# Kernel tuning notes

Hardware: AMD Instinct MI355X
Metric: run time of the kernel (lower is better)

Reference implementation:

```python
import jax, jax.numpy as jnp
import numpy as np

HID = 2048   # hidden_size
NH = 32      # num_heads (== num_kv_heads)
HD = 64      # head_dim
TH, TW = 8, 16     # tile sizes (tile numel 128, flex-attention block)
WH, WW = 16, 32    # window sizes in tokens
SCALE = 1.0 / np.sqrt(HD)


def _kv_tile_index(h_dim, w_dim):
    # Static tile-level sliding window (mirrors sliding_window_tile_2d mask_mod).
    Ht, Wt = h_dim // TH, w_dim // TW          # tile grid
    wh, ww = WH // TH, WW // TW                # window in tile units
    lr, rr = wh // 2, wh // 2 + (wh % 2 - 1)
    lc, rc = ww // 2, ww // 2 + (ww % 2 - 1)
    cr = np.clip(np.arange(Ht), lr, Ht - 1 - rr)   # clamped window center rows
    cc = np.clip(np.arange(Wt), lc, Wt - 1 - rc)
    rows = cr[:, None] + np.arange(-lr, rr + 1)[None, :]   # [Ht, wh]
    cols = cc[:, None] + np.arange(-lc, rc + 1)[None, :]   # [Wt, ww]
    idx = rows[:, None, :, None] * Wt + cols[None, :, None, :]  # [Ht,Wt,wh,ww]
    return idx.reshape(Ht * Wt, wh * ww)


def _tile_order(x, h_dim, w_dim):
    # seq layout (nth th ntw tw) -> [B, NH, n_tiles, TH*TW, HD]  (the einops rearrange)
    B, S, _ = x.shape
    nth, ntw = h_dim // TH, w_dim // TW
    x = x.reshape(B, nth, TH, ntw, TW, NH, HD)
    x = x.transpose(0, 5, 1, 3, 2, 4, 6)  # b h nth ntw th tw d
    return x.reshape(B, NH, nth * ntw, TH * TW, HD)


def setup_inputs() -> dict:
    key = jax.random.key(0)
    ks = jax.random.split(key, 5)
    B, hd, wd = 2, 64, 64
    S = hd * wd
    sc = 1.0 / np.sqrt(HID)
    return {
        "hidden_states": jax.random.normal(ks[0], (B, S, HID), jnp.float32),
        "Wq": jax.random.normal(ks[1], (HID, NH * HD), jnp.float32) * sc,
        "Wk": jax.random.normal(ks[2], (HID, NH * HD), jnp.float32) * sc,
        "Wv": jax.random.normal(ks[3], (HID, NH * HD), jnp.float32) * sc,
        "Wo": jax.random.normal(ks[4], (NH * HD, HID), jnp.float32) * sc,
        "h_dim": hd,
        "w_dim": wd,
    }


def reference(hidden_states, Wq, Wk, Wv, Wo, h_dim, w_dim):
    B, S, _ = hidden_states.shape
    q = _tile_order(hidden_states @ Wq, h_dim, w_dim)
    k = _tile_order(hidden_states @ Wk, h_dim, w_dim)
    v = _tile_order(hidden_states @ Wv, h_dim, w_dim)
    kv_tiles = jnp.asarray(_kv_tile_index(h_dim, w_dim))  # [T, nw] static
    T, nw = kv_tiles.shape
    tn = TH * TW
    # gather the allowed kv tiles per query tile (block-sparse structure)
    kg = k[:, :, kv_tiles].reshape(B, NH, T, nw * tn, HD)
    vg = v[:, :, kv_tiles].reshape(B, NH, T, nw * tn, HD)
    s = jnp.einsum('bhtqd,bhtkd->bhtqk', q, kg) * SCALE  # [B,H,T,128,nw*128]
    p = jax.nn.softmax(s, axis=-1)
    o = jnp.einsum('bhtqk,bhtkd->bhtqd', p, vg)
    # back to (nth th ntw tw) token order, then output projection
    nth, ntw = h_dim // TH, w_dim // TW
    o = o.reshape(B, NH, nth, ntw, TH, TW, HD)
    o = o.transpose(0, 2, 4, 3, 5, 1, 6).reshape(B, S, NH * HD)
    return o @ Wo
```

## Files before the change

### kernel.cpp

```cpp
#include <hip/hip_runtime.h>
#include <math.h>

typedef _Float16 f16;
typedef _Float16 f16x2 __attribute__((ext_vector_type(2)));
typedef _Float16 f16x4 __attribute__((ext_vector_type(4)));
typedef _Float16 f16x8 __attribute__((ext_vector_type(8)));
typedef float f32x4 __attribute__((ext_vector_type(4)));

#define K_HID 2048
#define N_SEQ 4096
#define N_BATCH 2
#define M_ROWS 8192

__device__ __forceinline__ void gl2lds16(const f16* g, f16* l) {
  auto gp = (const __attribute__((address_space(1))) unsigned*)(unsigned long long)(uintptr_t)g;
  auto lp = (__attribute__((address_space(3))) unsigned*)(unsigned)(uintptr_t)l;
  __builtin_amdgcn_global_load_lds(gp, lp, 16, 0, 0);
}

__global__ __launch_bounds__(256) void cvt_f32_to_f16(const float* __restrict__ x,
                                                      f16* __restrict__ y, int n) {
  int i = (blockIdx.x * 256 + threadIdx.x) * 8;
  if (i >= n) return;
  float4 a = *(const float4*)(x + i);
  float4 b = *(const float4*)(x + i + 4);
  f16x8 o;
  o[0] = (f16)a.x; o[1] = (f16)a.y; o[2] = (f16)a.z; o[3] = (f16)a.w;
  o[4] = (f16)b.x; o[5] = (f16)b.y; o[6] = (f16)b.z; o[7] = (f16)b.w;
  *(f16x8*)(y + i) = o;
}

__global__ __launch_bounds__(256) void transpose_cvt(const float* __restrict__ W0,
                                                     const float* __restrict__ W1,
                                                     const float* __restrict__ W2,
                                                     const float* __restrict__ W3,
                                                     f16* __restrict__ WT) {
  const float* W = (blockIdx.z == 0) ? W0 : (blockIdx.z == 1) ? W1
                 : (blockIdx.z == 2) ? W2 : W3;
  f16* Wt = WT + (size_t)blockIdx.z * K_HID * K_HID;
  __shared__ float tile[32][33];
  int bx = blockIdx.x * 32;
  int by = blockIdx.y * 32;
  int x = threadIdx.x & 31;
  int y = threadIdx.x >> 5;
  for (int i = 0; i < 32; i += 8)
    tile[y + i][x] = W[(size_t)(by + y + i) * K_HID + bx + x];
  __syncthreads();
  for (int i = 0; i < 32; i += 8)
    Wt[(size_t)(bx + y + i) * K_HID + by + x] = (f16)tile[x][y + i];
}

template <typename OutT>
__global__ __launch_bounds__(512, 2) void gemm_bt(const f16* __restrict__ A,
                                                  const f16* __restrict__ BtBase,
                                                  OutT* __restrict__ CBase,
                                                  int M, int N, int Kd,
                                                  size_t bzStride, size_t czStride) {
  const f16* Bt = BtBase + bzStride * blockIdx.z;
  OutT* C = CBase + czStride * blockIdx.z;
  __shared__ f16 sA[2][256 * 64];
  __shared__ f16 sB[2][256 * 64];
  int tid = threadIdx.x;
  int lane = tid & 63, wave = tid >> 6;
  int quad = lane >> 4, l16 = lane & 15;
  int mBase = blockIdx.y * 256, nBase = blockIdx.x * 256;
  int wm = (wave >> 2) * 128, wn = (wave & 3) * 64;

  f32x4 acc[8][4];
#pragma unroll
  for (int mf = 0; mf < 8; mf++)
#pragma unroll
    for (int nf = 0; nf < 4; nf++) acc[mf][nf] = (f32x4){0.f, 0.f, 0.f, 0.f};

  int r8 = lane >> 3;
  int csw = ((lane & 7) ^ r8) * 8;
  const f16* Ag = A + (size_t)(mBase + wave * 32 + r8) * Kd + csw;
  const f16* Bg = Bt + (size_t)(nBase + wave * 32 + r8) * Kd + csw;

  f16* lA0 = &sA[0][wave * 2048];
  f16* lA1 = &sA[1][wave * 2048];
  f16* lB0 = &sB[0][wave * 2048];
  f16* lB1 = &sB[1][wave * 2048];

#define STAGE_A(dst, t)                                                  \
  { _Pragma("unroll") for (int q = 0; q < 4; ++q)                        \
      gl2lds16(Ag + (size_t)(q * 8) * Kd + (size_t)(t) * 64, (dst) + q * 512); }
#define STAGE_B(dst, t)                                                  \
  { _Pragma("unroll") for (int q = 0; q < 4; ++q)                        \
      gl2lds16(Bg + (size_t)(q * 8) * Kd + (size_t)(t) * 64, (dst) + q * 512); }

  int aRow = (wm + l16) * 64;
  int bRow = (wn + l16) * 64;
  int c0 = (quad ^ (l16 & 7)) * 8;
  int c1 = c0 ^ 32;

  const int NT = Kd >> 6;
  STAGE_A(lA0, 0);
  STAGE_B(lB0, 0);

  const f16* sAc = &sA[0][0]; const f16* sAo = &sA[1][0];
  const f16* sBc = &sB[0][0]; const f16* sBo = &sB[1][0];
  f16* lAn = lA1; f16* lAo = lA0;
  f16* lBn = lB1; f16* lBo = lB0;

  for (int t = 0; t < NT; ++t) {
    if (t + 1 < NT) {
      STAGE_A(lAn, t + 1);
      asm volatile("s_waitcnt vmcnt(4)" ::: "memory");
    } else {
      asm volatile("s_waitcnt vmcnt(0)" ::: "memory");
    }
    __builtin_amdgcn_s_barrier();
    __builtin_amdgcn_sched_barrier(0);

    f16x8 bf[4][2], af[4][2];
#pragma unroll
    for (int nf = 0; nf < 4; nf++) {
      bf[nf][0] = *(const f16x8*)&sBc[bRow + nf * 1024 + c0];
      bf[nf][1] = *(const f16x8*)&sBc[bRow + nf * 1024 + c1];
    }
#pragma unroll
    for (int mf = 0; mf < 4; mf++) {
      af[mf][0] = *(const f16x8*)&sAc[aRow + mf * 1024 + c0];
      af[mf][1] = *(const f16x8*)&sAc[aRow + mf * 1024 + c1];
    }
    __builtin_amdgcn_s_setprio(1);
#pragma unroll
    for (int mf = 0; mf < 4; mf++)
#pragma unroll
      for (int nf = 0; nf < 4; nf++) {
        acc[mf][nf] = __builtin_amdgcn_mfma_f32_16x16x32_f16(af[mf][0], bf[nf][0], acc[mf][nf], 0, 0, 0);
        acc[mf][nf] = __builtin_amdgcn_mfma_f32_16x16x32_f16(af[mf][1], bf[nf][1], acc[mf][nf], 0, 0, 0);
      }
    __builtin_amdgcn_s_setprio(0);

    if (t + 1 < NT) STAGE_B(lBn, t + 1);

#pragma unroll
    for (int mf = 0; mf < 4; mf++) {
      af[mf][0] = *(const f16x8*)&sAc[aRow + 4096 + mf * 1024 + c0];
      af[mf][1] = *(const f16x8*)&sAc[aRow + 4096 + mf * 1024 + c1];
    }
    __builtin_amdgcn_s_setprio(1);
#pragma unroll
    for (int mf = 0; mf < 4; mf++)
#pragma unroll
      for (int nf = 0; nf < 4; nf++) {
        acc[mf + 4][nf] = __builtin_amdgcn_mfma_f32_16x16x32_f16(af[mf][0], bf[nf][0], acc[mf + 4][nf], 0, 0, 0);
        acc[mf + 4][nf] = __builtin_amdgcn_mfma_f32_16x16x32_f16(af[mf][1], bf[nf][1], acc[mf + 4][nf], 0, 0, 0);
      }
    __builtin_amdgcn_s_setprio(0);
    __builtin_amdgcn_sched_barrier(0);
    __builtin_amdgcn_s_barrier();

    { const f16* tt;
      tt = sAc; sAc = sAo; sAo = tt;
      tt = sBc; sBc = sBo; sBo = tt; }
    { f16* tt;
      tt = lAn; lAn = lAo; lAo = tt;
      tt = lBn; lBn = lBo; lBo = tt; }
  }
#undef STAGE_A
#undef STAGE_B

#pragma unroll
  for (int mf = 0; mf < 8; mf++) {
    int row = mBase + wm + mf * 16 + quad * 4;
#pragma unroll
    for (int nf = 0; nf < 4; nf++) {
      int col = nBase + wn + nf * 16 + l16;
      OutT* Cp = C + (size_t)row * N + col;
#pragma unroll
      for (int r = 0; r < 4; r++) Cp[(size_t)r * N] = (OutT)acc[mf][nf][r];
    }
  }
}

__global__ __launch_bounds__(256) void attn_kernel(const f16* __restrict__ Q,
                                                   const f16* __restrict__ Kg,
                                                   const f16* __restrict__ V,
                                                   f16* __restrict__ O) {
  __shared__ f16 sK[64 * 72];
  __shared__ f16 sVt[64 * 72];
  __shared__ f16 sPt[128 * 72];

  int t = blockIdx.x, h = blockIdx.y, b = blockIdx.z;
  int nth_i = t >> 2, ntw_i = t & 3;
  int tid = threadIdx.x;
  int lane = tid & 63, wave = tid >> 6;
  int quad = lane >> 4, l16 = lane & 15;
  const size_t bstride = (size_t)N_SEQ * K_HID;
  const f16* Qb = Q + (size_t)b * bstride + h * 64;
  const f16* Kb = Kg + (size_t)b * bstride + h * 64;
  const f16* Vb = V + (size_t)b * bstride + h * 64;

  const float SC2 = 0.18033688f;

  for (int i = tid; i < 1024; i += 256) {
    int qr = i >> 3, dc = (i & 7) * 8;
    int s = (nth_i * 8 + (qr >> 4)) * 64 + ntw_i * 16 + (qr & 15);
    *(float4*)&sPt[qr * 72 + dc] = *(const float4*)&Qb[(size_t)s * K_HID + dc];
  }
  __syncthreads();

  f16x8 qf[2][2];
#pragma unroll
  for (int qs = 0; qs < 2; qs++)
#pragma unroll
    for (int kk = 0; kk < 2; kk++)
      qf[qs][kk] = *(const f16x8*)&sPt[(wave * 32 + qs * 16 + l16) * 72 + kk * 32 + quad * 8];

  f32x4 oacc[2][4];
#pragma unroll
  for (int qs = 0; qs < 2; qs++)
#pragma unroll
    for (int dt = 0; dt < 4; dt++) oacc[qs][dt] = (f32x4){0.f, 0.f, 0.f, 0.f};
  float mrow[2] = {-1e30f, -1e30f};
  float lrow[2] = {0.f, 0.f};

  int cr = min(max(nth_i, 1), 7);
  int cc = min(max(ntw_i, 1), 3);

  for (int c = 0; c < 8; c++) {
    int kt = c >> 1, half = c & 1;
    int ti = cr - 1 + (kt >> 1), tj = cc - 1 + (kt & 1);
    for (int i = tid; i < 512; i += 256) {
      int kl = i >> 3, dc = (i & 7) * 8;
      int kr = half * 64 + kl;
      int s = (ti * 8 + (kr >> 4)) * 64 + tj * 16 + (kr & 15);
      *(float4*)&sK[kl * 72 + dc] = *(const float4*)&Kb[(size_t)s * K_HID + dc];
    }
    {
      int pr = tid >> 3, dc = (tid & 7) * 8;
      int k0 = pr * 2;
      int kr0 = half * 64 + k0, kr1 = kr0 + 1;
      int s0 = (ti * 8 + (kr0 >> 4)) * 64 + tj * 16 + (kr0 & 15);
      int s1 = (ti * 8 + (kr1 >> 4)) * 64 + tj * 16 + (kr1 & 15);
      f16x8 v0 = *(const f16x8*)&Vb[(size_t)s0 * K_HID + dc];
      f16x8 v1 = *(const f16x8*)&Vb[(size_t)s1 * K_HID + dc];
      int swc = k0 ^ dc;
#pragma unroll
      for (int j = 0; j < 8; j++) {
        f16x2 pv; pv[0] = v0[j]; pv[1] = v1[j];
        *(f16x2*)&sVt[(dc + j) * 72 + swc] = pv;
      }
    }
    __syncthreads();

    f32x4 sacc[2][4];
#pragma unroll
    for (int qs = 0; qs < 2; qs++)
#pragma unroll
      for (int ks = 0; ks < 4; ks++) sacc[qs][ks] = (f32x4){0.f, 0.f, 0.f, 0.f};
#pragma unroll
    for (int ks = 0; ks < 4; ks++) {
      f16x8 kf0 = *(const f16x8*)&sK[(ks * 16 + l16) * 72 + quad * 8];
      f16x8 kf1 = *(const f16x8*)&sK[(ks * 16 + l16) * 72 + 32 + quad * 8];
#pragma unroll
      for (int qs = 0; qs < 2; qs++) {
        sacc[qs][ks] = __builtin_amdgcn_mfma_f32_16x16x32_f16(kf0, qf[qs][0], sacc[qs][ks], 0, 0, 0);
        sacc[qs][ks] = __builtin_amdgcn_mfma_f32_16x16x32_f16(kf1, qf[qs][1], sacc[qs][ks], 0, 0, 0);
      }
    }

#pragma unroll
    for (int qs = 0; qs < 2; qs++) {
      float mx = sacc[qs][0][0];
#pragma unroll
      for (int ks = 0; ks < 4; ks++)
#pragma unroll
        for (int r = 0; r < 4; r++) mx = fmaxf(mx, sacc[qs][ks][r]);
      mx = fmaxf(mx, __shfl_xor(mx, 16, 64));
      mx = fmaxf(mx, __shfl_xor(mx, 32, 64));
      mx *= SC2;
      float mold = mrow[qs];
      float mnew = fmaxf(mold, mx);
      mrow[qs] = mnew;
      float alpha = exp2f(mold - mnew);
      lrow[qs] *= alpha;
#pragma unroll
      for (int dt = 0; dt < 4; dt++)
#pragma unroll
        for (int r = 0; r < 4; r++) oacc[qs][dt][r] *= alpha;
      float ls = 0.f;
      int qrow = (wave * 32 + qs * 16 + l16) * 72;
#pragma unroll
      for (int ks = 0; ks < 4; ks++) {
        f16x4 pk;
#pragma unroll
        for (int r = 0; r < 4; r++) {
          float p = exp2f(sacc[qs][ks][r] * SC2 - mnew);
          ls += p;
          pk[r] = (f16)p;
        }
        *(f16x4*)&sPt[qrow + ks * 16 + quad * 4] = pk;
      }
      lrow[qs] += ls;
    }
    __syncthreads();

#pragma unroll
    for (int kk = 0; kk < 2; kk++) {
      f16x8 pf[2];
#pragma unroll
      for (int qs = 0; qs < 2; qs++)
        pf[qs] = *(const f16x8*)&sPt[(wave * 32 + qs * 16 + l16) * 72 + kk * 32 + quad * 8];
#pragma unroll
      for (int dt = 0; dt < 4; dt++) {
        int d = dt * 16 + l16;
        f16x8 vf = *(const f16x8*)&sVt[d * 72 + ((kk * 32 + quad * 8) ^ (d & 56))];
#pragma unroll
        for (int qs = 0; qs < 2; qs++)
          oacc[qs][dt] = __builtin_amdgcn_mfma_f32_16x16x32_f16(vf, pf[qs], oacc[qs][dt], 0, 0, 0);
      }
    }
    __syncthreads();
  }

  f16* Ob = O + (size_t)b * bstride + h * 64;
#pragma unroll
  for (int qs = 0; qs < 2; qs++) {
    float l = lrow[qs];
    l += __shfl_xor(l, 16, 64);
    l += __shfl_xor(l, 32, 64);
    float inv = 1.0f / l;
    int q = wave * 32 + qs * 16 + l16;
    int s = (nth_i * 8 + (q >> 4)) * 64 + ntw_i * 16 + (q & 15);
#pragma unroll
    for (int dt = 0; dt < 4; dt++) {
      f16x4 ok;
#pragma unroll
      for (int r = 0; r < 4; r++) ok[r] = (f16)(oacc[qs][dt][r] * inv);
      *(f16x4*)&Ob[(size_t)s * K_HID + dt * 16 + quad * 4] = ok;
    }
  }
}

extern "C" void kernel_launch(void* const* d_in, const int* in_sizes, int n_in,
                              void* d_out, int out_size, void* d_ws, size_t ws_size,
                              hipStream_t stream) {
  const float* hs = (const float*)d_in[0];
  const float* Wq = (const float*)d_in[1];
  const float* Wk = (const float*)d_in[2];
  const float* Wv = (const float*)d_in[3];
  const float* Wo = (const float*)d_in[4];
  float* out = (float*)d_out;

  char* ws = (char*)d_ws;
  const size_t WELEM = (size_t)K_HID * K_HID;
  const size_t XELEM = (size_t)M_ROWS * K_HID;
  f16* WT = (f16*)ws;  ws += 4 * WELEM * sizeof(f16);
  f16* Xh = (f16*)ws;  ws += XELEM * sizeof(f16);
  f16* Qb = (f16*)ws;  ws += XELEM * sizeof(f16);
  f16* Kb = (f16*)ws;  ws += XELEM * sizeof(f16);
  f16* Vb = (f16*)ws;  ws += XELEM * sizeof(f16);
  f16* Ob = (f16*)ws;  ws += XELEM * sizeof(f16);

  cvt_f32_to_f16<<<(int)(XELEM / (256 * 8)), 256, 0, stream>>>(hs, Xh, (int)XELEM);
  transpose_cvt<<<dim3(64, 64, 4), 256, 0, stream>>>(Wq, Wk, Wv, Wo, WT);
  gemm_bt<f16><<<dim3(8, 32, 3), 512, 0, stream>>>(Xh, WT, Qb, M_ROWS, K_HID, K_HID,
                                                   WELEM, XELEM);
  attn_kernel<<<dim3(32, 32, 2), 256, 0, stream>>>(Qb, Kb, Vb, Ob);
  gemm_bt<float><<<dim3(8, 32, 1), 512, 0, stream>>>(Ob, WT + 3 * WELEM, out,
                                                     M_ROWS, K_HID, K_HID, 0, 0);
}
```

Measured before the change: 524.8 us.

## Split GEMM K-step into four quadrant phases with finer-grained global-to-LDS staging

```diff
diff --git a/kernel.cpp b/kernel.cpp
--- a/kernel.cpp
+++ b/kernel.cpp
@@ -74,20 +74,26 @@
 
   int r8 = lane >> 3;
   int csw = ((lane & 7) ^ r8) * 8;
-  const f16* Ag = A + (size_t)(mBase + wave * 32 + r8) * Kd + csw;
-  const f16* Bg = Bt + (size_t)(nBase + wave * 32 + r8) * Kd + csw;
-
-  f16* lA0 = &sA[0][wave * 2048];
-  f16* lA1 = &sA[1][wave * 2048];
-  f16* lB0 = &sB[0][wave * 2048];
-  f16* lB1 = &sB[1][wave * 2048];
-
-#define STAGE_A(dst, t)                                                  \
-  { _Pragma("unroll") for (int q = 0; q < 4; ++q)                        \
-      gl2lds16(Ag + (size_t)(q * 8) * Kd + (size_t)(t) * 64, (dst) + q * 512); }
-#define STAGE_B(dst, t)                                                  \
-  { _Pragma("unroll") for (int q = 0; q < 4; ++q)                        \
-      gl2lds16(Bg + (size_t)(q * 8) * Kd + (size_t)(t) * 64, (dst) + q * 512); }
+  int bA0 = wave, bA1 = wave + 16, bA2 = wave + 8, bA3 = wave + 24;
+  int bBb = (wave & 3) + ((wave >> 2) << 3);
+  int bB0 = bBb, bB1 = bBb + 16, bB2 = bBb + 4, bB3 = bBb + 20;
+  const f16* AgJ0 = A + (size_t)(mBase + bA0 * 8 + r8) * Kd + csw;
+  const f16* AgJ1 = A + (size_t)(mBase + bA1 * 8 + r8) * Kd + csw;
+  const f16* AgJ2 = A + (size_t)(mBase + bA2 * 8 + r8) * Kd + csw;
+  const f16* AgJ3 = A + (size_t)(mBase + bA3 * 8 + r8) * Kd + csw;
+  const f16* BgJ0 = Bt + (size_t)(nBase + bB0 * 8 + r8) * Kd + csw;
+  const f16* BgJ1 = Bt + (size_t)(nBase + bB1 * 8 + r8) * Kd + csw;
+  const f16* BgJ2 = Bt + (size_t)(nBase + bB2 * 8 + r8) * Kd + csw;
+  const f16* BgJ3 = Bt + (size_t)(nBase + bB3 * 8 + r8) * Kd + csw;
+
+#define STG_A01(buf, tt) { gl2lds16(AgJ0 + (size_t)(tt) * 64, (buf) + bA0 * 512); \
+                           gl2lds16(AgJ1 + (size_t)(tt) * 64, (buf) + bA1 * 512); }
+#define STG_A23(buf, tt) { gl2lds16(AgJ2 + (size_t)(tt) * 64, (buf) + bA2 * 512); \
+                           gl2lds16(AgJ3 + (size_t)(tt) * 64, (buf) + bA3 * 512); }
+#define STG_B01(buf, tt) { gl2lds16(BgJ0 + (size_t)(tt) * 64, (buf) + bB0 * 512); \
+                           gl2lds16(BgJ1 + (size_t)(tt) * 64, (buf) + bB1 * 512); }
+#define STG_B23(buf, tt) { gl2lds16(BgJ2 + (size_t)(tt) * 64, (buf) + bB2 * 512); \
+                           gl2lds16(BgJ3 + (size_t)(tt) * 64, (buf) + bB3 * 512); }
 
   int aRow = (wm + l16) * 64;
   int bRow = (wn + l16) * 64;
@@ -95,73 +101,113 @@
   int c1 = c0 ^ 32;
 
   const int NT = Kd >> 6;
-  STAGE_A(lA0, 0);
-  STAGE_B(lB0, 0);
-
-  const f16* sAc = &sA[0][0]; const f16* sAo = &sA[1][0];
-  const f16* sBc = &sB[0][0]; const f16* sBo = &sB[1][0];
-  f16* lAn = lA1; f16* lAo = lA0;
-  f16* lBn = lB1; f16* lBo = lB0;
+
+  f16* cA = &sA[0][0]; f16* nA = &sA[1][0];
+  f16* cB = &sB[0][0]; f16* nB = &sB[1][0];
+
+  STG_A01(cA, 0); STG_B01(cB, 0); STG_B23(cB, 0); STG_A23(cA, 0);
 
   for (int t = 0; t < NT; ++t) {
-    if (t + 1 < NT) {
-      STAGE_A(lAn, t + 1);
-      asm volatile("s_waitcnt vmcnt(4)" ::: "memory");
-    } else {
-      asm volatile("s_waitcnt vmcnt(0)" ::: "memory");
-    }
-    __builtin_amdgcn_s_barrier();
-    __builtin_amdgcn_sched_barrier(0);
-
-    f16x8 bf[4][2], af[4][2];
-#pragma unroll
-    for (int nf = 0; nf < 4; nf++) {
-      bf[nf][0] = *(const f16x8*)&sBc[bRow + nf * 1024 + c0];
-      bf[nf][1] = *(const f16x8*)&sBc[bRow + nf * 1024 + c1];
-    }
+    const bool pre = (t + 1 < NT);
+    f16x8 af[4][2], bf[2][2];
+    if (pre) STG_A01(nA, t + 1);
+    if (pre) asm volatile("s_waitcnt vmcnt(6)" ::: "memory");
+    else     asm volatile("s_waitcnt vmcnt(4)" ::: "memory");
+    __builtin_amdgcn_s_barrier();
+    __builtin_amdgcn_sched_barrier(0);
 #pragma unroll
     for (int mf = 0; mf < 4; mf++) {
-      af[mf][0] = *(const f16x8*)&sAc[aRow + mf * 1024 + c0];
-      af[mf][1] = *(const f16x8*)&sAc[aRow + mf * 1024 + c1];
-    }
+      af[mf][0] = *(const f16x8*)&cA[aRow + mf * 1024 + c0];
+      af[mf][1] = *(const f16x8*)&cA[aRow + mf * 1024 + c1];
+    }
+#pragma unroll
+    for (int nf = 0; nf < 2; nf++) {
+      bf[nf][0] = *(const f16x8*)&cB[bRow + nf * 1024 + c0];
+      bf[nf][1] = *(const f16x8*)&cB[bRow + nf * 1024 + c1];
+    }
+    asm volatile("s_waitcnt lgkmcnt(0)" ::: "memory");
+    __builtin_amdgcn_sched_barrier(0);
     __builtin_amdgcn_s_setprio(1);
 #pragma unroll
     for (int mf = 0; mf < 4; mf++)
 #pragma unroll
-      for (int nf = 0; nf < 4; nf++) {
+      for (int nf = 0; nf < 2; nf++) {
         acc[mf][nf] = __builtin_amdgcn_mfma_f32_16x16x32_f16(af[mf][0], bf[nf][0], acc[mf][nf], 0, 0, 0);
         acc[mf][nf] = __builtin_amdgcn_mfma_f32_16x16x32_f16(af[mf][1], bf[nf][1], acc[mf][nf], 0, 0, 0);
       }
     __builtin_amdgcn_s_setprio(0);
-
-    if (t + 1 < NT) STAGE_B(lBn, t + 1);
-
+    __builtin_amdgcn_s_barrier();
+    if (pre) STG_B01(nB, t + 1);
+    if (pre) asm volatile("s_waitcnt vmcnt(6)" ::: "memory");
+    else     asm volatile("s_waitcnt vmcnt(2)" ::: "memory");
+    __builtin_amdgcn_s_barrier();
+    __builtin_amdgcn_sched_barrier(0);
+#pragma unroll
+    for (int nf = 0; nf < 2; nf++) {
+      bf[nf][0] = *(const f16x8*)&cB[bRow + (nf + 2) * 1024 + c0];
+      bf[nf][1] = *(const f16x8*)&cB[bRow + (nf + 2) * 1024 + c1];
+    }
+    asm volatile("s_waitcnt lgkmcnt(0)" ::: "memory");
+    __builtin_amdgcn_sched_barrier(0);
+    __builtin_amdgcn_s_setprio(1);
+#pragma unroll
+    for (int mf = 0; mf < 4; mf++)
+#pragma unroll
+      for (int nf = 0; nf < 2; nf++) {
+        acc[mf][nf + 2] = __builtin_amdgcn_mfma_f32_16x16x32_f16(af[mf][0], bf[nf][0], acc[mf][nf + 2], 0, 0, 0);
+        acc[mf][nf + 2] = __builtin_amdgcn_mfma_f32_16x16x32_f16(af[mf][1], bf[nf][1], acc[mf][nf + 2], 0, 0, 0);
+      }
+    __builtin_amdgcn_s_setprio(0);
+    __builtin_amdgcn_s_barrier();
+    if (pre) STG_B23(nB, t + 1);
+    if (pre) asm volatile("s_waitcnt vmcnt(6)" ::: "memory");
+    else     asm volatile("s_waitcnt vmcnt(0)" ::: "memory");
+    __builtin_amdgcn_s_barrier();
+    __builtin_amdgcn_sched_barrier(0);
 #pragma unroll
     for (int mf = 0; mf < 4; mf++) {
-      af[mf][0] = *(const f16x8*)&sAc[aRow + 4096 + mf * 1024 + c0];
-      af[mf][1] = *(const f16x8*)&sAc[aRow + 4096 + mf * 1024 + c1];
-    }
+      af[mf][0] = *(const f16x8*)&cA[aRow + (mf + 4) * 1024 + c0];
+      af[mf][1] = *(const f16x8*)&cA[aRow + (mf + 4) * 1024 + c1];
+    }
+    asm volatile("s_waitcnt lgkmcnt(0)" ::: "memory");
+    __builtin_amdgcn_sched_barrier(0);
     __builtin_amdgcn_s_setprio(1);
 #pragma unroll
     for (int mf = 0; mf < 4; mf++)
 #pragma unroll
-      for (int nf = 0; nf < 4; nf++) {
+      for (int nf = 0; nf < 2; nf++) {
+        acc[mf + 4][nf + 2] = __builtin_amdgcn_mfma_f32_16x16x32_f16(af[mf][0], bf[nf][0], acc[mf + 4][nf + 2], 0, 0, 0);
+        acc[mf + 4][nf + 2] = __builtin_amdgcn_mfma_f32_16x16x32_f16(af[mf][1], bf[nf][1], acc[mf + 4][nf + 2], 0, 0, 0);
+      }
+    __builtin_amdgcn_s_setprio(0);
+    __builtin_amdgcn_s_barrier();
+    if (pre) STG_A23(nA, t + 1);
+    __builtin_amdgcn_s_barrier();
+    __builtin_amdgcn_sched_barrier(0);
+#pragma unroll
+    for (int nf = 0; nf < 2; nf++) {
+      bf[nf][0] = *(const f16x8*)&cB[bRow + nf * 1024 + c0];
+      bf[nf][1] = *(const f16x8*)&cB[bRow + nf * 1024 + c1];
+    }
+    asm volatile("s_waitcnt lgkmcnt(0)" ::: "memory");
+    __builtin_amdgcn_sched_barrier(0);
+    __builtin_amdgcn_s_setprio(1);
+#pragma unroll
+    for (int mf = 0; mf < 4; mf++)
+#pragma unroll
+      for (int nf = 0; nf < 2; nf++) {
         acc[mf + 4][nf] = __builtin_amdgcn_mfma_f32_16x16x32_f16(af[mf][0], bf[nf][0], acc[mf + 4][nf], 0, 0, 0);
         acc[mf + 4][nf] = __builtin_amdgcn_mfma_f32_16x16x32_f16(af[mf][1], bf[nf][1], acc[mf + 4][nf], 0, 0, 0);
       }
     __builtin_amdgcn_s_setprio(0);
-    __builtin_amdgcn_sched_barrier(0);
-    __builtin_amdgcn_s_barrier();
-
-    { const f16* tt;
-      tt = sAc; sAc = sAo; sAo = tt;
-      tt = sBc; sBc = sBo; sBo = tt; }
-    { f16* tt;
-      tt = lAn; lAn = lAo; lAo = tt;
-      tt = lBn; lBn = lBo; lBo = tt; }
+    __builtin_amdgcn_s_barrier();
+    { f16* tt = cA; cA = nA; nA = tt; }
+    { f16* tt = cB; cB = nB; nB = tt; }
   }
-#undef STAGE_A
-#undef STAGE_B
+#undef STG_A01
+#undef STG_A23
+#undef STG_B01
+#undef STG_B23
 
 #pragma unroll
   for (int mf = 0; mf < 8; mf++) {
```

Measured after the change: 521.5 us. No clear change (-0.6%).

## Prefetch next K/V chunk into registers while computing current attention chunk

Applied to the files above, without the earlier changes.

```diff
diff --git a/kernel.cpp b/kernel.cpp
--- a/kernel.cpp
+++ b/kernel.cpp
@@ -196,11 +196,46 @@
 
   const float SC2 = 0.18033688f;
 
+  int cr = min(max(nth_i, 1), 7);
+  int cc = min(max(ntw_i, 1), 3);
+
+  int klK = tid >> 3, dcK = (tid & 7) * 8;
+  int k0V = (tid >> 3) * 2, dcV = (tid & 7) * 8;
+  int swcV = k0V ^ dcV;
+  float4 krg0, krg1; f16x8 v0r, v1r;
+
+#define KV_LOAD(cx) {                                                         \
+    int c_ = (cx);                                                            \
+    int ti_ = cr - 1 + (c_ >> 2), tj_ = cc - 1 + ((c_ >> 1) & 1);             \
+    int hb_ = (c_ & 1) * 64;                                                  \
+    int kr_ = hb_ + klK;                                                      \
+    int s_ = (ti_ * 8 + (kr_ >> 4)) * 64 + tj_ * 16 + (kr_ & 15);             \
+    krg0 = *(const float4*)&Kb[(size_t)s_ * K_HID + dcK];                     \
+    kr_ = hb_ + klK + 32;                                                     \
+    s_ = (ti_ * 8 + (kr_ >> 4)) * 64 + tj_ * 16 + (kr_ & 15);                 \
+    krg1 = *(const float4*)&Kb[(size_t)s_ * K_HID + dcK];                     \
+    kr_ = hb_ + k0V;                                                          \
+    s_ = (ti_ * 8 + (kr_ >> 4)) * 64 + tj_ * 16 + (kr_ & 15);                 \
+    v0r = *(const f16x8*)&Vb[(size_t)s_ * K_HID + dcV];                       \
+    kr_ = hb_ + k0V + 1;                                                      \
+    s_ = (ti_ * 8 + (kr_ >> 4)) * 64 + tj_ * 16 + (kr_ & 15);                 \
+    v1r = *(const f16x8*)&Vb[(size_t)s_ * K_HID + dcV];                       \
+  }
+#define KV_WRITE() {                                                          \
+    *(float4*)&sK[klK * 72 + dcK] = krg0;                                     \
+    *(float4*)&sK[(klK + 32) * 72 + dcK] = krg1;                              \
+    _Pragma("unroll") for (int j = 0; j < 8; j++) {                           \
+      f16x2 pv_; pv_[0] = v0r[j]; pv_[1] = v1r[j];                            \
+      *(f16x2*)&sVt[(dcV + j) * 72 + swcV] = pv_;                             \
+    }                                                                         \
+  }
+
   for (int i = tid; i < 1024; i += 256) {
     int qr = i >> 3, dc = (i & 7) * 8;
     int s = (nth_i * 8 + (qr >> 4)) * 64 + ntw_i * 16 + (qr & 15);
     *(float4*)&sPt[qr * 72 + dc] = *(const float4*)&Qb[(size_t)s * K_HID + dc];
   }
+  KV_LOAD(0);
   __syncthreads();
 
   f16x8 qf[2][2];
@@ -209,6 +244,8 @@
 #pragma unroll
     for (int kk = 0; kk < 2; kk++)
       qf[qs][kk] = *(const f16x8*)&sPt[(wave * 32 + qs * 16 + l16) * 72 + kk * 32 + quad * 8];
+  KV_WRITE();
+  __syncthreads();
 
   f32x4 oacc[2][4];
 #pragma unroll
@@ -218,34 +255,9 @@
   float mrow[2] = {-1e30f, -1e30f};
   float lrow[2] = {0.f, 0.f};
 
-  int cr = min(max(nth_i, 1), 7);
-  int cc = min(max(ntw_i, 1), 3);
-
   for (int c = 0; c < 8; c++) {
-    int kt = c >> 1, half = c & 1;
-    int ti = cr - 1 + (kt >> 1), tj = cc - 1 + (kt & 1);
-    for (int i = tid; i < 512; i += 256) {
-      int kl = i >> 3, dc = (i & 7) * 8;
-      int kr = half * 64 + kl;
-      int s = (ti * 8 + (kr >> 4)) * 64 + tj * 16 + (kr & 15);
-      *(float4*)&sK[kl * 72 + dc] = *(const float4*)&Kb[(size_t)s * K_HID + dc];
-    }
-    {
-      int pr = tid >> 3, dc = (tid & 7) * 8;
-      int k0 = pr * 2;
-      int kr0 = half * 64 + k0, kr1 = kr0 + 1;
-      int s0 = (ti * 8 + (kr0 >> 4)) * 64 + tj * 16 + (kr0 & 15);
-      int s1 = (ti * 8 + (kr1 >> 4)) * 64 + tj * 16 + (kr1 & 15);
-      f16x8 v0 = *(const f16x8*)&Vb[(size_t)s0 * K_HID + dc];
-      f16x8 v1 = *(const f16x8*)&Vb[(size_t)s1 * K_HID + dc];
-      int swc = k0 ^ dc;
-#pragma unroll
-      for (int j = 0; j < 8; j++) {
-        f16x2 pv; pv[0] = v0[j]; pv[1] = v1[j];
-        *(f16x2*)&sVt[(dc + j) * 72 + swc] = pv;
-      }
-    }
-    __syncthreads();
+    if (c < 7) KV_LOAD(c + 1);
+    __builtin_amdgcn_sched_barrier(0);
 
     f32x4 sacc[2][4];
 #pragma unroll
@@ -297,7 +309,6 @@
       }
       lrow[qs] += ls;
     }
-    __syncthreads();
 
 #pragma unroll
     for (int kk = 0; kk < 2; kk++) {
@@ -315,7 +326,13 @@
       }
     }
     __syncthreads();
-  }
+    if (c < 7) {
+      KV_WRITE();
+      __syncthreads();
+    }
+  }
+#undef KV_LOAD
+#undef KV_WRITE
 
   f16* Ob = O + (size_t)b * bstride + h * 64;
 #pragma unroll
```

Result: no change. 527.3 us (+0.5%).
